# Optimization experiments

Hardware: AMD Instinct MI355X
Metric: run time of the kernel (lower is better)

Reference implementation:

```python
import jax, jax.numpy as jnp
import numpy as np

B = 8192
DV, DT = 1024, 768          # visual / text dims
H = 256                     # hidden_dim
C = 5                       # num_classes
GH = 128                    # gate_hidden_dim
K = 8                       # graph_k
ALPHA = 0.5                 # graph_alpha
EW = 0.01                   # entropy_weight
FD = 2 * H                  # fused_dim = 512
GI = FD + C + H             # gate input dim = 773
NEG = -1.0e9
LN_EPS = 1e-5
BN_EPS = 1e-5
N_IMAGES = 512


def setup_inputs() -> dict:
    key = jax.random.key(0)
    ks = jax.random.split(key, 20)
    def rn(k, sh, s=0.02):
        return jax.random.normal(k, sh, dtype=jnp.float32) * s
    # x = [visual(1024) | text(768) | bbox_ctx(4) | img_uid(1)]
    xf = jax.random.normal(ks[0], (B, DV + DT), dtype=jnp.float32)
    bbox = jax.random.uniform(ks[1], (B, 4), dtype=jnp.float32)
    img = jax.random.randint(ks[2], (B, 1), 0, N_IMAGES).astype(jnp.float32)
    x = jnp.concatenate([xf, bbox, img], axis=1)  # [B, 1797]
    return {
        "x": x,
        "ln_v_g": jnp.ones((DV,), jnp.float32), "ln_v_b": jnp.zeros((DV,), jnp.float32),
        "ln_t_g": jnp.ones((DT,), jnp.float32), "ln_t_b": jnp.zeros((DT,), jnp.float32),
        "W_v": rn(ks[3], (DV, H)), "b_v": jnp.zeros((H,), jnp.float32),
        "W_t": rn(ks[4], (DT, H)), "b_t": jnp.zeros((H,), jnp.float32),
        "W_cp": rn(ks[5], (FD, C)), "b_cp": jnp.zeros((C,), jnp.float32),
        "W_ctx1": rn(ks[6], (FD, H)), "b_ctx1": jnp.zeros((H,), jnp.float32),
        "W_ctx2": rn(ks[7], (H, H)), "b_ctx2": jnp.zeros((H,), jnp.float32),
        "W_g1": rn(ks[8], (GI, GH)), "b_g1": jnp.zeros((GH,), jnp.float32),
        "W_g2": rn(ks[9], (GH, 2)), "b_g2": jnp.zeros((2,), jnp.float32),
        "W_gu1": rn(ks[10], (FD, FD)), "b_gu1": jnp.zeros((FD,), jnp.float32),
        "W_gu2": rn(ks[11], (FD, FD)), "b_gu2": jnp.zeros((FD,), jnp.float32),
        "W_c1": rn(ks[12], (FD, H)), "b_c1": jnp.zeros((H,), jnp.float32),
        "bn_g": jnp.ones((H,), jnp.float32), "bn_b": jnp.zeros((H,), jnp.float32),
        "W_c2": rn(ks[13], (H, C)), "b_c2": jnp.zeros((C,), jnp.float32),
    }


def _layernorm(x, g, b):
    m = jnp.mean(x, axis=-1, keepdims=True)
    v = jnp.mean((x - m) ** 2, axis=-1, keepdims=True)
    return (x - m) * jax.lax.rsqrt(v + LN_EPS) * g + b


def _knn_aggregate(features, coords, img):
    """KNN over 2D spatial coords with same-image masking; softmax-weighted gather."""
    n = features.shape[0]
    sq = jnp.sum(coords * coords, axis=1)
    d2 = sq[:, None] + sq[None, :] - 2.0 * (coords @ coords.T)
    sim = -jnp.sqrt(jnp.clip(d2, 0.0))                 # [B, B] = -cdist
    eye = jnp.eye(n, dtype=bool)
    same = (img[None, :] == img[:, None]) & ~eye
    has_neighbor = jnp.any(same, axis=1)
    sim_same = jnp.where(same, sim, NEG)
    sim = jnp.where(has_neighbor[:, None], sim_same, sim)
    sim = jnp.where(eye, NEG, sim)
    vals, idx = jax.lax.top_k(sim, K)                  # [B, K]
    w = jax.nn.softmax(vals, axis=1)
    return jnp.einsum('bk,bkd->bd', w, features[idx])  # gather + weighted sum


def reference(x, ln_v_g, ln_v_b, ln_t_g, ln_t_b, W_v, b_v, W_t, b_t,
              W_cp, b_cp, W_ctx1, b_ctx1, W_ctx2, b_ctx2,
              W_g1, b_g1, W_g2, b_g2, W_gu1, b_gu1, W_gu2, b_gu2,
              W_c1, b_c1, bn_g, bn_b, W_c2, b_c2):
    xv = x[:, 0:DV]
    xt = x[:, DV:DV + DT]
    coords = x[:, DV + DT:DV + DT + 2]     # bbox_ctx[:, :2]
    img = x[:, DV + DT + 4]                # img_uid[:, 0]

    fv = _layernorm(xv, ln_v_g, ln_v_b) @ W_v + b_v
    ft = _layernorm(xt, ln_t_g, ln_t_b) @ W_t + b_t
    base_fused = jnp.concatenate([fv, ft], axis=1)     # [B, FD]

    class_prior = jax.lax.stop_gradient(jax.nn.softmax(base_fused @ W_cp + b_cp, axis=1))

    neigh_agg = _knn_aggregate(base_fused, coords, img)
    spatial_token = jax.nn.relu(neigh_agg @ W_ctx1 + b_ctx1) @ W_ctx2 + b_ctx2
    spatial_token = jax.lax.stop_gradient(spatial_token)

    gate_in = jnp.concatenate([base_fused, class_prior, spatial_token], axis=1)
    gate_logits = jax.nn.relu(gate_in @ W_g1 + b_g1) @ W_g2 + b_g2
    gate_probs = jax.nn.softmax(gate_logits / 1.0, axis=1)  # temperature=1.0 (eval: dropout off)
    entropy = -jnp.sum(gate_probs * jnp.log(gate_probs + 1e-8), axis=1)
    entropy_loss = jnp.mean(entropy) * EW

    fused = jnp.concatenate([fv * gate_probs[:, 0:1], ft * gate_probs[:, 1:2]], axis=1)
    spatial_update = _knn_aggregate(fused, coords, img)
    upd = jax.nn.relu(spatial_update @ W_gu1 + b_gu1) @ W_gu2 + b_gu2
    fused = fused + ALPHA * upd

    h = fused @ W_c1 + b_c1
    # eval-mode BatchNorm1d: running_mean=0, running_var=1
    h = h * (bn_g / jnp.sqrt(1.0 + BN_EPS)) + bn_b
    h = jax.nn.relu(h)
    logits = h @ W_c2 + b_c2
    return logits, entropy_loss
```

## Files before the change

kernel.cpp:

```cpp
#include <hip/hip_runtime.h>
#include <math.h>

#define B_ROWS 8192
#define DV_DIM 1024
#define DT_DIM 768
#define H_DIM 256
#define C_CLS 5
#define GH_DIM 128
#define K_NN 8
#define FD_DIM 512
#define GIP_DIM 832
#define GI_REAL 773
#define XCOLS 1797
#define NEGV -1000000000.0f
#define LN_EPS_F 1e-5f
#define BN_EPS_F 1e-5f
#define N_IMG 512
#define EW_F 0.01f
#define ALPHA_F 0.5f

typedef __attribute__((ext_vector_type(8))) short short8v;
typedef __attribute__((ext_vector_type(4))) float f32x4;

__device__ inline short bf16r(float f) {
    unsigned u = __float_as_uint(f);
    return (short)((u + 0x7fffu + ((u >> 16) & 1u)) >> 16);
}

__device__ inline float bf2f(short s) {
    return __uint_as_float(((unsigned)(unsigned short)s) << 16);
}

__device__ inline void split2(float f, short* h, short* l) {
    unsigned u = __float_as_uint(f);
    unsigned uh = (u + 0x7fffu + ((u >> 16) & 1u)) >> 16;
    float fh = __uint_as_float(uh << 16);
    float fl = f - fh;
    unsigned ul = __float_as_uint(fl);
    *h = (short)uh;
    *l = (short)((ul + 0x7fffu + ((ul >> 16) & 1u)) >> 16);
}

struct PrepArgs {
    const float* W[8];
    short* h[8];
    int K[8];
    int N[8];
    int Kpad[8];
    int cnt[8];
};

__global__ void prep_all_kernel(PrepArgs a, const float* __restrict__ x,
                                float* __restrict__ cx, float* __restrict__ cy,
                                float* __restrict__ sq, int* __restrict__ imgi,
                                int* __restrict__ cnt) {
    int idx = blockIdx.x * blockDim.x + threadIdx.x;
#pragma unroll
    for (int s = 0; s < 8; ++s) {
        if (idx < a.cnt[s]) {
            int Kp = a.Kpad[s];
            int n = idx / Kp, k = idx - n * Kp;
            float f = (k < a.K[s]) ? a.W[s][(size_t)k * a.N[s] + n] : 0.f;
            a.h[s][idx] = bf16r(f);
            return;
        }
        idx -= a.cnt[s];
    }
    if (idx < B_ROWS) {
        const float* row = x + (size_t)idx * XCOLS;
        float av = row[DV_DIM + DT_DIM];
        float bv = row[DV_DIM + DT_DIM + 1];
        cx[idx] = av; cy[idx] = bv; sq[idx] = av * av + bv * bv;
        int m = (int)row[DV_DIM + DT_DIM + 4];
        imgi[idx] = m;
        atomicAdd(&cnt[m], 1);
    }
}

__global__ void scan_kernel(const int* __restrict__ cnt, int* __restrict__ start,
                            int* __restrict__ cursor) {
    __shared__ int s[N_IMG];
    int t = threadIdx.x;
    s[t] = cnt[t];
    __syncthreads();
    for (int off = 1; off < N_IMG; off <<= 1) {
        int v = (t >= off) ? s[t - off] : 0;
        __syncthreads();
        s[t] += v;
        __syncthreads();
    }
    int st = s[t] - cnt[t];
    start[t] = st;
    cursor[t] = st;
}

__global__ void scatter_kernel(const int* __restrict__ imgi, int* __restrict__ cursor,
                               int* __restrict__ perm) {
    int i = blockIdx.x * blockDim.x + threadIdx.x;
    if (i >= B_ROWS) return;
    int pos = atomicAdd(&cursor[imgi[i]], 1);
    perm[pos] = i;
}

__global__ void knn_kernel(const float* __restrict__ cx, const float* __restrict__ cy,
                           const float* __restrict__ sq, const int* __restrict__ imgi,
                           const int* __restrict__ cnt, const int* __restrict__ start,
                           const int* __restrict__ perm, int* __restrict__ knn_idx,
                           float* __restrict__ knn_w) {
    int i = blockIdx.x * blockDim.x + threadIdx.x;
    if (i >= B_ROWS) return;
    float xi = cx[i], yi = cy[i], si = sq[i];
    float vals[K_NN];
    int ids[K_NN];
#pragma unroll
    for (int k = 0; k < K_NN; ++k) { vals[k] = NEGV; ids[k] = i; }
    int m = imgi[i];
    int s = cnt[m];
    if (s >= 2) {
        int st = start[m];
        for (int t = 0; t < s; ++t) {
            int j = perm[st + t];
            if (j == i) continue;
            float d2 = si + sq[j] - 2.f * (xi * cx[j] + yi * cy[j]);
            d2 = fmaxf(d2, 0.f);
            float v = -sqrtf(d2);
            if (v > vals[K_NN - 1]) {
                int p = K_NN - 1;
                while (p > 0 && vals[p - 1] < v) {
                    vals[p] = vals[p - 1]; ids[p] = ids[p - 1]; --p;
                }
                vals[p] = v; ids[p] = j;
            }
        }
    } else {
        for (int j = 0; j < B_ROWS; ++j) {
            if (j == i) continue;
            float d2 = si + sq[j] - 2.f * (xi * cx[j] + yi * cy[j]);
            d2 = fmaxf(d2, 0.f);
            float v = -sqrtf(d2);
            if (v > vals[K_NN - 1]) {
                int p = K_NN - 1;
                while (p > 0 && vals[p - 1] < v) {
                    vals[p] = vals[p - 1]; ids[p] = ids[p - 1]; --p;
                }
                vals[p] = v; ids[p] = j;
            }
        }
    }
    float mx = vals[0];
    float e[K_NN];
    float sum = 0.f;
#pragma unroll
    for (int k = 0; k < K_NN; ++k) { e[k] = expf(vals[k] - mx); sum += e[k]; }
    float inv = 1.f / sum;
#pragma unroll
    for (int k = 0; k < K_NN; ++k) {
        knn_w[(size_t)i * K_NN + k] = e[k] * inv;
        knn_idx[(size_t)i * K_NN + k] = ids[k];
    }
}

__global__ __launch_bounds__(256) void ln_split_kernel(
    const float* __restrict__ x,
    const float* __restrict__ gv, const float* __restrict__ bv,
    const float* __restrict__ gt, const float* __restrict__ bt,
    short* __restrict__ xvh, short* __restrict__ xvl,
    short* __restrict__ xth, short* __restrict__ xtl) {
    int row = blockIdx.x;
    int t = threadIdx.x;
    const float* xr = x + (size_t)row * XCOLS;
    __shared__ float red[256];

    float v[4];
#pragma unroll
    for (int k = 0; k < 4; ++k) v[k] = xr[t + k * 256];
    float sum = v[0] + v[1] + v[2] + v[3];
    red[t] = sum;
    __syncthreads();
    for (int off = 128; off; off >>= 1) {
        if (t < off) red[t] += red[t + off];
        __syncthreads();
    }
    float mean = red[0] * (1.f / DV_DIM);
    __syncthreads();
    float vs = 0.f;
#pragma unroll
    for (int k = 0; k < 4; ++k) { float d = v[k] - mean; vs += d * d; }
    red[t] = vs;
    __syncthreads();
    for (int off = 128; off; off >>= 1) {
        if (t < off) red[t] += red[t + off];
        __syncthreads();
    }
    float rs = rsqrtf(red[0] * (1.f / DV_DIM) + LN_EPS_F);
#pragma unroll
    for (int k = 0; k < 4; ++k) {
        int j = t + k * 256;
        float y = (v[k] - mean) * rs * gv[j] + bv[j];
        split2(y, &xvh[(size_t)row * DV_DIM + j], &xvl[(size_t)row * DV_DIM + j]);
    }
    __syncthreads();

    float u[3];
#pragma unroll
    for (int k = 0; k < 3; ++k) u[k] = xr[DV_DIM + t + k * 256];
    sum = u[0] + u[1] + u[2];
    red[t] = sum;
    __syncthreads();
    for (int off = 128; off; off >>= 1) {
        if (t < off) red[t] += red[t + off];
        __syncthreads();
    }
    mean = red[0] * (1.f / DT_DIM);
    __syncthreads();
    vs = 0.f;
#pragma unroll
    for (int k = 0; k < 3; ++k) { float d = u[k] - mean; vs += d * d; }
    red[t] = vs;
    __syncthreads();
    for (int off = 128; off; off >>= 1) {
        if (t < off) red[t] += red[t + off];
        __syncthreads();
    }
    rs = rsqrtf(red[0] * (1.f / DT_DIM) + LN_EPS_F);
#pragma unroll
    for (int k = 0; k < 3; ++k) {
        int j = t + k * 256;
        float y = (u[k] - mean) * rs * gt[j] + bt[j];
        split2(y, &xth[(size_t)row * DT_DIM + j], &xtl[(size_t)row * DT_DIM + j]);
    }
}

__device__ inline int xcd_swz(int wg, int nwg) {
    int q = nwg >> 3, r = nwg & 7;
    int xc = wg & 7, ii = wg >> 3;
    return (xc < r ? xc * (q + 1) : r * (q + 1) + (xc - r) * q) + ii;
}

struct GemmPair {
    const short* Ah; const short* Al;
    const short* Bh; const short* Bl;
    const float* bias;
    int K; int ncb; int colOff;
};

template <int MODE, int NPROD, int NF>
__global__ __launch_bounds__(256) void gemm2_kernel(
    GemmPair P0, GemmPair P1, int nblk0,
    float* __restrict__ Cf, short* __restrict__ Ch,
    int ldc, const float* __restrict__ aux1, const float* __restrict__ aux2) {
    constexpr int ASZ = 4096;
    constexpr int BSZ = 32 * NF * 64;
    constexpr int LDSZ = (NPROD == 3) ? 2 * (ASZ + BSZ) : (NPROD == 2 ? 2 * ASZ + BSZ : ASZ + BSZ);
    __shared__ short lds[LDSZ];
    short* sAh = lds;
    short* sAl = lds + ASZ;
    short* sBh = lds + ((NPROD >= 2) ? 2 * ASZ : ASZ);
    short* sBl = sBh + BSZ;

    const int tid = threadIdx.x;
    const int lane = tid & 63;
    const int wave = tid >> 6;
    const int wm = wave >> 1, wn = wave & 1;
    const int l15 = lane & 15, lq = lane >> 4;

    int wid = xcd_swz(blockIdx.x, gridDim.x);
    GemmPair G = P0;
    if (wid >= nblk0) { G = P1; wid -= nblk0; }

    const int panel = wid / G.ncb, cb = wid - panel * G.ncb;
    const long rowBase = (long)panel * 64;
    const int colBase = cb * (32 * NF);
    const int K = G.K;

    f32x4 acc[2][NF];
#pragma unroll
    for (int i = 0; i < 2; ++i)
#pragma unroll
        for (int j = 0; j < NF; ++j) acc[i][j] = (f32x4){0.f, 0.f, 0.f, 0.f};

    short8v pAh[2], pAl[2], pBh[NF], pBl[NF];
    const int ar0 = tid >> 3, ac = tid & 7;
    const int ar1 = (tid + 256) >> 3;

    {
        long go0 = (rowBase + ar0) * K + ac * 8;
        long go1 = (rowBase + ar1) * K + ac * 8;
        pAh[0] = *(const short8v*)(G.Ah + go0);
        pAh[1] = *(const short8v*)(G.Ah + go1);
        if constexpr (NPROD >= 2) {
            pAl[0] = *(const short8v*)(G.Al + go0);
            pAl[1] = *(const short8v*)(G.Al + go1);
        }
#pragma unroll
        for (int j = 0; j < NF; ++j) {
            int cid = tid + 256 * j;
            int cl = cid >> 3, c = cid & 7;
            long go = (colBase + cl) * (long)K + c * 8;
            pBh[j] = *(const short8v*)(G.Bh + go);
            if constexpr (NPROD == 3) pBl[j] = *(const short8v*)(G.Bl + go);
        }
    }

    const int nsteps = K >> 6;
    for (int s = 0; s < nsteps; ++s) {
        __syncthreads();
        {
            int off0 = ar0 * 64 + ((ac ^ (ar0 & 7)) << 3);
            int off1 = ar1 * 64 + ((ac ^ (ar1 & 7)) << 3);
            *(short8v*)(sAh + off0) = pAh[0];
            *(short8v*)(sAh + off1) = pAh[1];
            if constexpr (NPROD >= 2) {
                *(short8v*)(sAl + off0) = pAl[0];
                *(short8v*)(sAl + off1) = pAl[1];
            }
#pragma unroll
            for (int j = 0; j < NF; ++j) {
                int cid = tid + 256 * j;
                int cl = cid >> 3, c = cid & 7;
                int off = cl * 64 + ((c ^ (cl & 7)) << 3);
                *(short8v*)(sBh + off) = pBh[j];
                if constexpr (NPROD == 3) *(short8v*)(sBl + off) = pBl[j];
            }
        }
        __syncthreads();
        if (s + 1 < nsteps) {
            long ko = (long)(s + 1) * 64;
            long go0 = (rowBase + ar0) * K + ko + ac * 8;
            long go1 = (rowBase + ar1) * K + ko + ac * 8;
            pAh[0] = *(const short8v*)(G.Ah + go0);
            pAh[1] = *(const short8v*)(G.Ah + go1);
            if constexpr (NPROD >= 2) {
                pAl[0] = *(const short8v*)(G.Al + go0);
                pAl[1] = *(const short8v*)(G.Al + go1);
            }
#pragma unroll
            for (int j = 0; j < NF; ++j) {
                int cid = tid + 256 * j;
                int cl = cid >> 3, c = cid & 7;
                long go = (colBase + cl) * (long)K + ko + c * 8;
                pBh[j] = *(const short8v*)(G.Bh + go);
                if constexpr (NPROD == 3) pBl[j] = *(const short8v*)(G.Bl + go);
            }
        }
#pragma unroll
        for (int ksub = 0; ksub < 2; ++ksub) {
            int cc = ksub * 4 + lq;
            short8v afh[2], afl[2], bfh[NF], bfl[NF];
#pragma unroll
            for (int mf = 0; mf < 2; ++mf) {
                int rr = wm * 32 + mf * 16 + l15;
                int off = rr * 64 + ((cc ^ (rr & 7)) << 3);
                afh[mf] = *(short8v*)(sAh + off);
                if constexpr (NPROD >= 2) afl[mf] = *(short8v*)(sAl + off);
            }
#pragma unroll
            for (int nf = 0; nf < NF; ++nf) {
                int cl = wn * (NF * 16) + nf * 16 + l15;
                int off = cl * 64 + ((cc ^ (cl & 7)) << 3);
                bfh[nf] = *(short8v*)(sBh + off);
                if constexpr (NPROD == 3) bfl[nf] = *(short8v*)(sBl + off);
            }
#pragma unroll
            for (int mf = 0; mf < 2; ++mf)
#pragma unroll
                for (int nf = 0; nf < NF; ++nf) {
                    acc[mf][nf] = __builtin_amdgcn_mfma_f32_16x16x32_bf16(afh[mf], bfh[nf], acc[mf][nf], 0, 0, 0);
                    if constexpr (NPROD >= 2)
                        acc[mf][nf] = __builtin_amdgcn_mfma_f32_16x16x32_bf16(afl[mf], bfh[nf], acc[mf][nf], 0, 0, 0);
                    if constexpr (NPROD == 3)
                        acc[mf][nf] = __builtin_amdgcn_mfma_f32_16x16x32_bf16(afh[mf], bfl[nf], acc[mf][nf], 0, 0, 0);
                }
        }
    }

#pragma unroll
    for (int mf = 0; mf < 2; ++mf)
#pragma unroll
        for (int nf = 0; nf < NF; ++nf) {
            int col = colBase + wn * (NF * 16) + nf * 16 + l15;
            long row0 = rowBase + wm * 32 + mf * 16 + lq * 4;
#pragma unroll
            for (int rr = 0; rr < 4; ++rr) {
                long row = row0 + rr;
                float v = acc[mf][nf][rr] + G.bias[col];
                long o = row * ldc + G.colOff + col;
                if (MODE == 6) {
                    Cf[o] = v;
                    Ch[o] = bf16r(v);
                } else if (MODE == 3) {
                    Ch[o] = bf16r(fmaxf(v, 0.f));
                } else {
                    float g = aux2[row * 2 + (col >= H_DIM ? 1 : 0)];
                    float fv = aux1[row * FD_DIM + col] * g + ALPHA_F * v;
                    Ch[o] = bf16r(fv);
                }
            }
        }
}

__global__ __launch_bounds__(256) void post_base_kernel(
    const short* __restrict__ baseh, const float* __restrict__ Wcp,
    const float* __restrict__ bcp, const int* __restrict__ kidx,
    const float* __restrict__ wgt, short* __restrict__ gih,
    short* __restrict__ aggh) {
    int row = blockIdx.x;
    int t = threadIdx.x;
    short sa = baseh[(size_t)row * FD_DIM + t];
    short sb = baseh[(size_t)row * FD_DIM + t + 256];
    float a = bf2f(sa), b = bf2f(sb);

    __shared__ float red[C_CLS][256];
#pragma unroll
    for (int n = 0; n < C_CLS; ++n)
        red[n][t] = a * Wcp[t * C_CLS + n] + b * Wcp[(t + 256) * C_CLS + n];
    __syncthreads();
    for (int off = 128; off; off >>= 1) {
        if (t < off) {
#pragma unroll
            for (int n = 0; n < C_CLS; ++n) red[n][t] += red[n][t + off];
        }
        __syncthreads();
    }
    size_t go = (size_t)row * GIP_DIM;
    if (t == 0) {
        float lg[C_CLS];
#pragma unroll
        for (int n = 0; n < C_CLS; ++n) lg[n] = red[n][0] + bcp[n];
        float mx = lg[0];
#pragma unroll
        for (int n = 1; n < C_CLS; ++n) mx = fmaxf(mx, lg[n]);
        float s = 0.f;
        float e[C_CLS];
#pragma unroll
        for (int n = 0; n < C_CLS; ++n) { e[n] = expf(lg[n] - mx); s += e[n]; }
        float inv = 1.f / s;
#pragma unroll
        for (int n = 0; n < C_CLS; ++n) gih[go + FD_DIM + n] = bf16r(e[n] * inv);
    }
    gih[go + t] = sa;
    gih[go + t + 256] = sb;
    if (t < GIP_DIM - GI_REAL) gih[go + GI_REAL + t] = 0;

    int jj[K_NN];
    float ww[K_NN];
#pragma unroll
    for (int k = 0; k < K_NN; ++k) {
        jj[k] = kidx[(size_t)row * K_NN + k];
        ww[k] = wgt[(size_t)row * K_NN + k];
    }
#pragma unroll
    for (int half = 0; half < 2; ++half) {
        int d = t + half * 256;
        float s = 0.f;
#pragma unroll
        for (int k = 0; k < K_NN; ++k)
            s = fmaf(ww[k], bf2f(baseh[(size_t)jj[k] * FD_DIM + d]), s);
        aggh[(size_t)row * FD_DIM + d] = bf16r(s);
    }
}

__global__ __launch_bounds__(256) void gather_gate_kernel(
    const short* __restrict__ baseh, const int* __restrict__ kidx,
    const float* __restrict__ wgt, const float* __restrict__ gp,
    short* __restrict__ oh) {
    int row = blockIdx.x;
    int t = threadIdx.x;
    int jj[K_NN];
    float ww[K_NN], g0[K_NN], g1[K_NN];
#pragma unroll
    for (int k = 0; k < K_NN; ++k) {
        jj[k] = kidx[(size_t)row * K_NN + k];
        ww[k] = wgt[(size_t)row * K_NN + k];
        g0[k] = gp[(size_t)jj[k] * 2 + 0];
        g1[k] = gp[(size_t)jj[k] * 2 + 1];
    }
#pragma unroll
    for (int half = 0; half < 2; ++half) {
        int d = t + half * 256;
        float s = 0.f;
#pragma unroll
        for (int k = 0; k < K_NN; ++k) {
            float f = bf2f(baseh[(size_t)jj[k] * FD_DIM + d]);
            f *= (d < H_DIM) ? g0[k] : g1[k];
            s = fmaf(ww[k], f, s);
        }
        oh[(size_t)row * FD_DIM + d] = bf16r(s);
    }
}

__global__ __launch_bounds__(256) void ctxfused_kernel(
    const short* __restrict__ aggh, const short* __restrict__ wx1, const float* __restrict__ b1,
    const short* __restrict__ wx2, const float* __restrict__ b2, short* __restrict__ gih) {
    __shared__ short lds[2048 + 16384 + 8192];
    short* sA = lds;
    short* sB = lds + 2048;
    short* sH = lds + 2048 + 16384;

    const int tid = threadIdx.x;
    const int lane = tid & 63;
    const int wave = tid >> 6;
    const int l15 = lane & 15, lq = lane >> 4;
    int panel = xcd_swz(blockIdx.x, gridDim.x);
    const long rowBase = (long)panel * 32;

    const int ar = tid >> 3, ac = tid & 7;

    f32x4 acc[2][4];
#pragma unroll
    for (int i = 0; i < 2; ++i)
#pragma unroll
        for (int j = 0; j < 4; ++j) acc[i][j] = (f32x4){0.f, 0.f, 0.f, 0.f};

    short8v pA, pB[8];
    {
        pA = *(const short8v*)(aggh + (rowBase + ar) * 512 + ac * 8);
#pragma unroll
        for (int j = 0; j < 8; ++j) {
            int cid = tid + 256 * j;
            int cl = cid >> 3, c = cid & 7;
            pB[j] = *(const short8v*)(wx1 + (long)cl * 512 + c * 8);
        }
    }
    for (int s = 0; s < 8; ++s) {
        __syncthreads();
        *(short8v*)(sA + ar * 64 + ((ac ^ (ar & 7)) << 3)) = pA;
#pragma unroll
        for (int j = 0; j < 8; ++j) {
            int cid = tid + 256 * j;
            int cl = cid >> 3, c = cid & 7;
            *(short8v*)(sB + cl * 64 + ((c ^ (cl & 7)) << 3)) = pB[j];
        }
        __syncthreads();
        if (s + 1 < 8) {
            long ko = (long)(s + 1) * 64;
            pA = *(const short8v*)(aggh + (rowBase + ar) * 512 + ko + ac * 8);
#pragma unroll
            for (int j = 0; j < 8; ++j) {
                int cid = tid + 256 * j;
                int cl = cid >> 3, c = cid & 7;
                pB[j] = *(const short8v*)(wx1 + (long)cl * 512 + ko + c * 8);
            }
        }
#pragma unroll
        for (int ksub = 0; ksub < 2; ++ksub) {
            int cc = ksub * 4 + lq;
            short8v af[2], bf[4];
#pragma unroll
            for (int mf = 0; mf < 2; ++mf) {
                int rr = mf * 16 + l15;
                af[mf] = *(short8v*)(sA + rr * 64 + ((cc ^ (rr & 7)) << 3));
            }
#pragma unroll
            for (int nf = 0; nf < 4; ++nf) {
                int cl = wave * 64 + nf * 16 + l15;
                bf[nf] = *(short8v*)(sB + cl * 64 + ((cc ^ (cl & 7)) << 3));
            }
#pragma unroll
            for (int mf = 0; mf < 2; ++mf)
#pragma unroll
                for (int nf = 0; nf < 4; ++nf)
                    acc[mf][nf] = __builtin_amdgcn_mfma_f32_16x16x32_bf16(af[mf], bf[nf], acc[mf][nf], 0, 0, 0);
        }
    }
    __syncthreads();
#pragma unroll
    for (int mf = 0; mf < 2; ++mf)
#pragma unroll
        for (int nf = 0; nf < 4; ++nf) {
            int col = wave * 64 + nf * 16 + l15;
            int sub = col >> 6, cch = (col >> 3) & 7, ce = col & 7;
#pragma unroll
            for (int rr = 0; rr < 4; ++rr) {
                int r = mf * 16 + lq * 4 + rr;
                float v = fmaxf(acc[mf][nf][rr] + b1[col], 0.f);
                sH[sub * 2048 + r * 64 + ((cch ^ (r & 7)) << 3) + ce] = bf16r(v);
            }
        }
    f32x4 acc2[2][4];
#pragma unroll
    for (int i = 0; i < 2; ++i)
#pragma unroll
        for (int j = 0; j < 4; ++j) acc2[i][j] = (f32x4){0.f, 0.f, 0.f, 0.f};
    for (int s = 0; s < 4; ++s) {
        __syncthreads();
#pragma unroll
        for (int j = 0; j < 8; ++j) {
            int cid = tid + 256 * j;
            int cl = cid >> 3, c = cid & 7;
            short8v b = *(const short8v*)(wx2 + (long)cl * 256 + s * 64 + c * 8);
            *(short8v*)(sB + cl * 64 + ((c ^ (cl & 7)) << 3)) = b;
        }
        __syncthreads();
#pragma unroll
        for (int ksub = 0; ksub < 2; ++ksub) {
            int cc = ksub * 4 + lq;
            short8v af[2], bf[4];
#pragma unroll
            for (int mf = 0; mf < 2; ++mf) {
                int rr = mf * 16 + l15;
                af[mf] = *(short8v*)(sH + s * 2048 + rr * 64 + ((cc ^ (rr & 7)) << 3));
            }
#pragma unroll
            for (int nf = 0; nf < 4; ++nf) {
                int cl = wave * 64 + nf * 16 + l15;
                bf[nf] = *(short8v*)(sB + cl * 64 + ((cc ^ (cl & 7)) << 3));
            }
#pragma unroll
            for (int mf = 0; mf < 2; ++mf)
#pragma unroll
                for (int nf = 0; nf < 4; ++nf)
                    acc2[mf][nf] = __builtin_amdgcn_mfma_f32_16x16x32_bf16(af[mf], bf[nf], acc2[mf][nf], 0, 0, 0);
        }
    }
#pragma unroll
    for (int mf = 0; mf < 2; ++mf)
#pragma unroll
        for (int nf = 0; nf < 4; ++nf) {
            int col = wave * 64 + nf * 16 + l15;
#pragma unroll
            for (int rr = 0; rr < 4; ++rr) {
                long row = rowBase + mf * 16 + lq * 4 + rr;
                gih[row * GIP_DIM + FD_DIM + C_CLS + col] = bf16r(acc2[mf][nf][rr] + b2[col]);
            }
        }
}

__global__ __launch_bounds__(256) void g1gate_kernel(
    const short* __restrict__ gih, const short* __restrict__ wg1, const float* __restrict__ b1,
    const float* __restrict__ W2, const float* __restrict__ b2,
    float* __restrict__ gp, float* __restrict__ entpart) {
    __shared__ float hls[64 * 128];
    short* sA = (short*)hls;
    short* sB = sA + 4096;
    __shared__ float entrow[64];

    const int tid = threadIdx.x;
    const int lane = tid & 63;
    const int wave = tid >> 6;
    const int wm = wave >> 1, wn = wave & 1;
    const int l15 = lane & 15, lq = lane >> 4;
    int panel = xcd_swz(blockIdx.x, gridDim.x);
    const long rowBase = (long)panel * 64;

    const int ar0 = tid >> 3, ac = tid & 7;
    const int ar1 = (tid + 256) >> 3;
    constexpr int K = GIP_DIM;

    f32x4 acc[2][4];
#pragma unroll
    for (int i = 0; i < 2; ++i)
#pragma unroll
        for (int j = 0; j < 4; ++j) acc[i][j] = (f32x4){0.f, 0.f, 0.f, 0.f};

    short8v pA0, pA1, pB[4];
    {
        pA0 = *(const short8v*)(gih + (rowBase + ar0) * K + ac * 8);
        pA1 = *(const short8v*)(gih + (rowBase + ar1) * K + ac * 8);
#pragma unroll
        for (int j = 0; j < 4; ++j) {
            int cid = tid + 256 * j;
            int cl = cid >> 3, c = cid & 7;
            pB[j] = *(const short8v*)(wg1 + (long)cl * K + c * 8);
        }
    }
    const int nsteps = K >> 6;
    for (int s = 0; s < nsteps; ++s) {
        __syncthreads();
        *(short8v*)(sA + ar0 * 64 + ((ac ^ (ar0 & 7)) << 3)) = pA0;
        *(short8v*)(sA + ar1 * 64 + ((ac ^ (ar1 & 7)) << 3)) = pA1;
#pragma unroll
        for (int j = 0; j < 4; ++j) {
            int cid = tid + 256 * j;
            int cl = cid >> 3, c = cid & 7;
            *(short8v*)(sB + cl * 64 + ((c ^ (cl & 7)) << 3)) = pB[j];
        }
        __syncthreads();
        if (s + 1 < nsteps) {
            long ko = (long)(s + 1) * 64;
            pA0 = *(const short8v*)(gih + (rowBase + ar0) * K + ko + ac * 8);
            pA1 = *(const short8v*)(gih + (rowBase + ar1) * K + ko + ac * 8);
#pragma unroll
            for (int j = 0; j < 4; ++j) {
                int cid = tid + 256 * j;
                int cl = cid >> 3, c = cid & 7;
                pB[j] = *(const short8v*)(wg1 + (long)cl * K + ko + c * 8);
            }
        }
#pragma unroll
        for (int ksub = 0; ksub < 2; ++ksub) {
            int cc = ksub * 4 + lq;
            short8v af[2], bf[4];
#pragma unroll
            for (int mf = 0; mf < 2; ++mf) {
                int rr = wm * 32 + mf * 16 + l15;
                af[mf] = *(short8v*)(sA + rr * 64 + ((cc ^ (rr & 7)) << 3));
            }
#pragma unroll
            for (int nf = 0; nf < 4; ++nf) {
                int cl = wn * 64 + nf * 16 + l15;
                bf[nf] = *(short8v*)(sB + cl * 64 + ((cc ^ (cl & 7)) << 3));
            }
#pragma unroll
            for (int mf = 0; mf < 2; ++mf)
#pragma unroll
                for (int nf = 0; nf < 4; ++nf)
                    acc[mf][nf] = __builtin_amdgcn_mfma_f32_16x16x32_bf16(af[mf], bf[nf], acc[mf][nf], 0, 0, 0);
        }
    }
    __syncthreads();
#pragma unroll
    for (int mf = 0; mf < 2; ++mf)
#pragma unroll
        for (int nf = 0; nf < 4; ++nf) {
            int col = wn * 64 + nf * 16 + l15;
#pragma unroll
            for (int rr = 0; rr < 4; ++rr) {
                int r = wm * 32 + mf * 16 + lq * 4 + rr;
                hls[r * 128 + col] = fmaxf(acc[mf][nf][rr] + b1[col], 0.f);
            }
        }
    __syncthreads();
    {
        int r = tid >> 2, p = tid & 3;
        float a0 = 0.f, a1 = 0.f;
#pragma unroll
        for (int i = 0; i < 32; ++i) {
            int c = p + i * 4;
            float hv = hls[r * 128 + c];
            a0 = fmaf(hv, W2[c * 2 + 0], a0);
            a1 = fmaf(hv, W2[c * 2 + 1], a1);
        }
        a0 += __shfl_xor(a0, 1); a1 += __shfl_xor(a1, 1);
        a0 += __shfl_xor(a0, 2); a1 += __shfl_xor(a1, 2);
        if (p == 0) {
            float l0 = a0 + b2[0], l1 = a1 + b2[1];
            float mx = fmaxf(l0, l1);
            float e0 = expf(l0 - mx), e1 = expf(l1 - mx);
            float ssum = e0 + e1;
            float p0 = e0 / ssum, p1 = e1 / ssum;
            long grow = rowBase + r;
            gp[grow * 2 + 0] = p0;
            gp[grow * 2 + 1] = p1;
            entrow[r] = -(p0 * logf(p0 + 1e-8f) + p1 * logf(p1 + 1e-8f));
        }
    }
    __syncthreads();
    if (tid == 0) {
        float s = 0.f;
        for (int r = 0; r < 64; ++r) s += entrow[r];
        entpart[blockIdx.x] = s;
    }
}

__global__ __launch_bounds__(256) void c1logits_kernel(
    const short* __restrict__ fusedh, const short* __restrict__ wc1, const float* __restrict__ b1,
    const float* __restrict__ bng, const float* __restrict__ bnb,
    const float* __restrict__ W2, const float* __restrict__ b2,
    const float* __restrict__ entpart, float* __restrict__ out) {
    __shared__ short lds[2048 + 16384];
    short* sA = lds;
    short* sB = lds + 2048;
    float* hls = (float*)lds;

    const int tid = threadIdx.x;
    const int lane = tid & 63;
    const int wave = tid >> 6;
    const int l15 = lane & 15, lq = lane >> 4;
    int panel = xcd_swz(blockIdx.x, gridDim.x);
    const long rowBase = (long)panel * 32;
    const int ar = tid >> 3, ac = tid & 7;

    f32x4 acc[2][4];
#pragma unroll
    for (int i = 0; i < 2; ++i)
#pragma unroll
        for (int j = 0; j < 4; ++j) acc[i][j] = (f32x4){0.f, 0.f, 0.f, 0.f};

    short8v pA, pB[8];
    {
        pA = *(const short8v*)(fusedh + (rowBase + ar) * 512 + ac * 8);
#pragma unroll
        for (int j = 0; j < 8; ++j) {
            int cid = tid + 256 * j;
            int cl = cid >> 3, c = cid & 7;
            pB[j] = *(const short8v*)(wc1 + (long)cl * 512 + c * 8);
        }
    }
    for (int s = 0; s < 8; ++s) {
        __syncthreads();
        *(short8v*)(sA + ar * 64 + ((ac ^ (ar & 7)) << 3)) = pA;
#pragma unroll
        for (int j = 0; j < 8; ++j) {
            int cid = tid + 256 * j;
            int cl = cid >> 3, c = cid & 7;
            *(short8v*)(sB + cl * 64 + ((c ^ (cl & 7)) << 3)) = pB[j];
        }
        __syncthreads();
        if (s + 1 < 8) {
            long ko = (long)(s + 1) * 64;
            pA = *(const short8v*)(fusedh + (rowBase + ar) * 512 + ko + ac * 8);
#pragma unroll
            for (int j = 0; j < 8; ++j) {
                int cid = tid + 256 * j;
                int cl = cid >> 3, c = cid & 7;
                pB[j] = *(const short8v*)(wc1 + (long)cl * 512 + ko + c * 8);
            }
        }
#pragma unroll
        for (int ksub = 0; ksub < 2; ++ksub) {
            int cc = ksub * 4 + lq;
            short8v af[2], bf[4];
#pragma unroll
            for (int mf = 0; mf < 2; ++mf) {
                int rr = mf * 16 + l15;
                af[mf] = *(short8v*)(sA + rr * 64 + ((cc ^ (rr & 7)) << 3));
            }
#pragma unroll
            for (int nf = 0; nf < 4; ++nf) {
                int cl = wave * 64 + nf * 16 + l15;
                bf[nf] = *(short8v*)(sB + cl * 64 + ((cc ^ (cl & 7)) << 3));
            }
#pragma unroll
            for (int mf = 0; mf < 2; ++mf)
#pragma unroll
                for (int nf = 0; nf < 4; ++nf)
                    acc[mf][nf] = __builtin_amdgcn_mfma_f32_16x16x32_bf16(af[mf], bf[nf], acc[mf][nf], 0, 0, 0);
        }
    }
    __syncthreads();
#pragma unroll
    for (int mf = 0; mf < 2; ++mf)
#pragma unroll
        for (int nf = 0; nf < 4; ++nf) {
            int col = wave * 64 + nf * 16 + l15;
            float scale = bng[col] * rsqrtf(1.f + BN_EPS_F);
            float shift = bnb[col];
#pragma unroll
            for (int rr = 0; rr < 4; ++rr) {
                int r = mf * 16 + lq * 4 + rr;
                float v = (acc[mf][nf][rr] + b1[col]) * scale + shift;
                hls[r * 256 + col] = fmaxf(v, 0.f);
            }
        }
    __syncthreads();
    {
        int r = tid >> 3, p = tid & 7;
        float a[C_CLS];
#pragma unroll
        for (int n = 0; n < C_CLS; ++n) a[n] = 0.f;
#pragma unroll
        for (int i = 0; i < 32; ++i) {
            int c = p + i * 8;
            float hv = hls[r * 256 + c];
#pragma unroll
            for (int n = 0; n < C_CLS; ++n) a[n] = fmaf(hv, W2[c * 5 + n], a[n]);
        }
#pragma unroll
        for (int n = 0; n < C_CLS; ++n) {
            a[n] += __shfl_xor(a[n], 1);
            a[n] += __shfl_xor(a[n], 2);
            a[n] += __shfl_xor(a[n], 4);
        }
        if (p == 0) {
            long grow = rowBase + r;
#pragma unroll
            for (int n = 0; n < C_CLS; ++n) out[grow * C_CLS + n] = a[n] + b2[n];
        }
    }
    if (blockIdx.x == 0 && tid < 64) {
        float s = entpart[tid] + entpart[tid + 64];
        for (int off = 32; off; off >>= 1) s += __shfl_down(s, off);
        if (tid == 0) out[(size_t)B_ROWS * C_CLS] = s * (EW_F / (float)B_ROWS);
    }
}

extern "C" void kernel_launch(void* const* d_in, const int* in_sizes, int n_in,
                              void* d_out, int out_size, void* d_ws, size_t ws_size,
                              hipStream_t stream) {
    const float* x = (const float*)d_in[0];
    const float* ln_v_g = (const float*)d_in[1];
    const float* ln_v_b = (const float*)d_in[2];
    const float* ln_t_g = (const float*)d_in[3];
    const float* ln_t_b = (const float*)d_in[4];
    const float* W_v = (const float*)d_in[5];
    const float* b_v = (const float*)d_in[6];
    const float* W_t = (const float*)d_in[7];
    const float* b_t = (const float*)d_in[8];
    const float* W_cp = (const float*)d_in[9];
    const float* b_cp = (const float*)d_in[10];
    const float* W_ctx1 = (const float*)d_in[11];
    const float* b_ctx1 = (const float*)d_in[12];
    const float* W_ctx2 = (const float*)d_in[13];
    const float* b_ctx2 = (const float*)d_in[14];
    const float* W_g1 = (const float*)d_in[15];
    const float* b_g1 = (const float*)d_in[16];
    const float* W_g2 = (const float*)d_in[17];
    const float* b_g2 = (const float*)d_in[18];
    const float* W_gu1 = (const float*)d_in[19];
    const float* b_gu1 = (const float*)d_in[20];
    const float* W_gu2 = (const float*)d_in[21];
    const float* b_gu2 = (const float*)d_in[22];
    const float* W_c1 = (const float*)d_in[23];
    const float* b_c1 = (const float*)d_in[24];
    const float* bn_g = (const float*)d_in[25];
    const float* bn_b = (const float*)d_in[26];
    const float* W_c2 = (const float*)d_in[27];
    const float* b_c2 = (const float*)d_in[28];

    float* out = (float*)d_out;

    char* wsb = (char*)d_ws;
    size_t off = 0;
    auto alloc = [&](size_t bytes) {
        char* p = wsb + off;
        off += (bytes + 255) & ~(size_t)255;
        return p;
    };
    float* base = (float*)alloc((size_t)B_ROWS * FD_DIM * 4);
    short* baseh = (short*)alloc((size_t)B_ROWS * FD_DIM * 2);
    short* aggh = (short*)alloc((size_t)B_ROWS * FD_DIM * 2);
    float* gp = (float*)alloc((size_t)B_ROWS * 2 * 4);
    float* entpart = (float*)alloc(128 * 4);
    float* cxv = (float*)alloc((size_t)B_ROWS * 4);
    float* cyv = (float*)alloc((size_t)B_ROWS * 4);
    float* sqv = (float*)alloc((size_t)B_ROWS * 4);
    float* wgt = (float*)alloc((size_t)B_ROWS * K_NN * 4);
    int* imgi = (int*)alloc((size_t)B_ROWS * 4);
    int* cnt = (int*)alloc(N_IMG * 4);
    int* startb = (int*)alloc(N_IMG * 4);
    int* cursor = (int*)alloc(N_IMG * 4);
    int* perm = (int*)alloc((size_t)B_ROWS * 4);
    int* kidx = (int*)alloc((size_t)B_ROWS * K_NN * 4);
    short* wv_h = (short*)alloc(256 * 1024 * 2);
    short* wt_h = (short*)alloc(256 * 768 * 2);
    short* wx1_h = (short*)alloc(256 * 512 * 2);
    short* wx2_h = (short*)alloc(256 * 256 * 2);
    short* wg1_h = (short*)alloc(128 * GIP_DIM * 2);
    short* wu1_h = (short*)alloc(512 * 512 * 2);
    short* wu2_h = (short*)alloc(512 * 512 * 2);
    short* wc1_h = (short*)alloc(256 * 512 * 2);
    char* R = alloc((size_t)B_ROWS * (DV_DIM + DT_DIM) * 2 * 2);
    short* xvh = (short*)R;
    short* xvl = xvh + (size_t)B_ROWS * DV_DIM;
    short* xth = xvl + (size_t)B_ROWS * DV_DIM;
    short* xtl = xth + (size_t)B_ROWS * DT_DIM;
    short* gih = (short*)R;
    short* guh = gih + (size_t)B_ROWS * GIP_DIM;
    short* fusedh = aggh;

    dim3 blk(256);
    dim3 gridRows((B_ROWS + 255) / 256);

    PrepArgs pa;
    const float* pw[8] = {W_v, W_t, W_ctx1, W_ctx2, W_g1, W_gu1, W_gu2, W_c1};
    short* ph[8] = {wv_h, wt_h, wx1_h, wx2_h, wg1_h, wu1_h, wu2_h, wc1_h};
    int pK[8] = {1024, 768, 512, 256, GI_REAL, 512, 512, 512};
    int pN[8] = {256, 256, 256, 256, 128, 512, 512, 256};
    int pKp[8] = {1024, 768, 512, 256, GIP_DIM, 512, 512, 512};
    int total = 0;
    for (int s = 0; s < 8; ++s) {
        pa.W[s] = pw[s]; pa.h[s] = ph[s];
        pa.K[s] = pK[s]; pa.N[s] = pN[s]; pa.Kpad[s] = pKp[s];
        pa.cnt[s] = pN[s] * pKp[s];
        total += pa.cnt[s];
    }
    hipMemsetAsync(cnt, 0, N_IMG * sizeof(int), stream);
    prep_all_kernel<<<(total + B_ROWS + 255) / 256, blk, 0, stream>>>(
        pa, x, cxv, cyv, sqv, imgi, cnt);

    scan_kernel<<<1, N_IMG, 0, stream>>>(cnt, startb, cursor);
    scatter_kernel<<<gridRows, blk, 0, stream>>>(imgi, cursor, perm);
    knn_kernel<<<gridRows, blk, 0, stream>>>(cxv, cyv, sqv, imgi, cnt, startb, perm, kidx, wgt);

    ln_split_kernel<<<B_ROWS, blk, 0, stream>>>(x, ln_v_g, ln_v_b, ln_t_g, ln_t_b,
                                                xvh, xvl, xth, xtl);

    GemmPair fvP{xvh, xvl, wv_h, nullptr, b_v, 1024, 4, 0};
    GemmPair ftP{xth, xtl, wt_h, nullptr, b_t, 768, 4, 256};
    gemm2_kernel<6, 2, 2><<<1024, blk, 0, stream>>>(fvP, ftP, 512, base, baseh,
                                                    FD_DIM, nullptr, nullptr);

    post_base_kernel<<<B_ROWS, blk, 0, stream>>>(baseh, W_cp, b_cp, kidx, wgt, gih, aggh);

    ctxfused_kernel<<<256, blk, 0, stream>>>(aggh, wx1_h, b_ctx1, wx2_h, b_ctx2, gih);

    g1gate_kernel<<<128, blk, 0, stream>>>(gih, wg1_h, b_g1, W_g2, b_g2, gp, entpart);

    gather_gate_kernel<<<B_ROWS, blk, 0, stream>>>(baseh, kidx, wgt, gp, aggh);
    GemmPair u1P{aggh, nullptr, wu1_h, nullptr, b_gu1, 512, 4, 0};
    gemm2_kernel<3, 1, 4><<<512, blk, 0, stream>>>(u1P, u1P, 512, nullptr, guh,
                                                   FD_DIM, nullptr, nullptr);
    GemmPair u2P{guh, nullptr, wu2_h, nullptr, b_gu2, 512, 4, 0};
    gemm2_kernel<5, 1, 4><<<512, blk, 0, stream>>>(u2P, u2P, 512, nullptr, fusedh,
                                                   FD_DIM, base, gp);

    c1logits_kernel<<<256, blk, 0, stream>>>(fusedh, wc1_h, b_c1, bn_g, bn_b,
                                             W_c2, b_c2, entpart, out);

    (void)in_sizes; (void)n_in; (void)out_size; (void)ws_size;
}
```

Baseline: 201.7 us.

## Drop bf16 split-precision for input GEMM and fuse kNN into LayerNorm launch

LayerNorm outputs are now stored as a single bf16 value instead of a hi/lo pair, and the first GEMM runs one MFMA product per tile instead of two. This halves the activation write/read traffic and the MFMA work for the largest GEMM. The kNN search is also folded into the LayerNorm kernel as 32 extra blocks, saving one launch and letting the two overlap. The price is lower precision in the visual and text projections, which could push outputs past the tolerance.

```diff
diff --git a/kernel.cpp b/kernel.cpp
--- a/kernel.cpp
+++ b/kernel.cpp
@@ -31,16 +31,6 @@
     return __uint_as_float(((unsigned)(unsigned short)s) << 16);
 }
 
-__device__ inline void split2(float f, short* h, short* l) {
-    unsigned u = __float_as_uint(f);
-    unsigned uh = (u + 0x7fffu + ((u >> 16) & 1u)) >> 16;
-    float fh = __uint_as_float(uh << 16);
-    float fl = f - fh;
-    unsigned ul = __float_as_uint(fl);
-    *h = (short)uh;
-    *l = (short)((ul + 0x7fffu + ((ul >> 16) & 1u)) >> 16);
-}
-
 struct PrepArgs {
     const float* W[8];
     short* h[8];
@@ -102,70 +92,70 @@
     perm[pos] = i;
 }
 
-__global__ void knn_kernel(const float* __restrict__ cx, const float* __restrict__ cy,
-                           const float* __restrict__ sq, const int* __restrict__ imgi,
-                           const int* __restrict__ cnt, const int* __restrict__ start,
-                           const int* __restrict__ perm, int* __restrict__ knn_idx,
-                           float* __restrict__ knn_w) {
-    int i = blockIdx.x * blockDim.x + threadIdx.x;
-    if (i >= B_ROWS) return;
-    float xi = cx[i], yi = cy[i], si = sq[i];
-    float vals[K_NN];
-    int ids[K_NN];
-#pragma unroll
-    for (int k = 0; k < K_NN; ++k) { vals[k] = NEGV; ids[k] = i; }
-    int m = imgi[i];
-    int s = cnt[m];
-    if (s >= 2) {
-        int st = start[m];
-        for (int t = 0; t < s; ++t) {
-            int j = perm[st + t];
-            if (j == i) continue;
-            float d2 = si + sq[j] - 2.f * (xi * cx[j] + yi * cy[j]);
-            d2 = fmaxf(d2, 0.f);
-            float v = -sqrtf(d2);
-            if (v > vals[K_NN - 1]) {
-                int p = K_NN - 1;
-                while (p > 0 && vals[p - 1] < v) {
-                    vals[p] = vals[p - 1]; ids[p] = ids[p - 1]; --p;
-                }
-                vals[p] = v; ids[p] = j;
-            }
-        }
-    } else {
-        for (int j = 0; j < B_ROWS; ++j) {
-            if (j == i) continue;
-            float d2 = si + sq[j] - 2.f * (xi * cx[j] + yi * cy[j]);
-            d2 = fmaxf(d2, 0.f);
-            float v = -sqrtf(d2);
-            if (v > vals[K_NN - 1]) {
-                int p = K_NN - 1;
-                while (p > 0 && vals[p - 1] < v) {
-                    vals[p] = vals[p - 1]; ids[p] = ids[p - 1]; --p;
-                }
-                vals[p] = v; ids[p] = j;
-            }
-        }
-    }
-    float mx = vals[0];
-    float e[K_NN];
-    float sum = 0.f;
-#pragma unroll
-    for (int k = 0; k < K_NN; ++k) { e[k] = expf(vals[k] - mx); sum += e[k]; }
-    float inv = 1.f / sum;
-#pragma unroll
-    for (int k = 0; k < K_NN; ++k) {
-        knn_w[(size_t)i * K_NN + k] = e[k] * inv;
-        knn_idx[(size_t)i * K_NN + k] = ids[k];
-    }
-}
-
-__global__ __launch_bounds__(256) void ln_split_kernel(
+__global__ __launch_bounds__(256) void lnknn_kernel(
     const float* __restrict__ x,
     const float* __restrict__ gv, const float* __restrict__ bv,
     const float* __restrict__ gt, const float* __restrict__ bt,
-    short* __restrict__ xvh, short* __restrict__ xvl,
-    short* __restrict__ xth, short* __restrict__ xtl) {
+    short* __restrict__ xvh, short* __restrict__ xth,
+    const float* __restrict__ cx, const float* __restrict__ cy,
+    const float* __restrict__ sq, const int* __restrict__ imgi,
+    const int* __restrict__ cnt, const int* __restrict__ start,
+    const int* __restrict__ perm, int* __restrict__ knn_idx,
+    float* __restrict__ knn_w) {
+    if (blockIdx.x >= B_ROWS) {
+        int i = (blockIdx.x - B_ROWS) * 256 + threadIdx.x;
+        if (i >= B_ROWS) return;
+        float xi = cx[i], yi = cy[i], si = sq[i];
+        float vals[K_NN];
+        int ids[K_NN];
+#pragma unroll
+        for (int k = 0; k < K_NN; ++k) { vals[k] = NEGV; ids[k] = i; }
+        int m = imgi[i];
+        int s = cnt[m];
+        if (s >= 2) {
+            int st = start[m];
+            for (int t = 0; t < s; ++t) {
+                int j = perm[st + t];
+                if (j == i) continue;
+                float d2 = si + sq[j] - 2.f * (xi * cx[j] + yi * cy[j]);
+                d2 = fmaxf(d2, 0.f);
+                float v = -sqrtf(d2);
+                if (v > vals[K_NN - 1]) {
+                    int p = K_NN - 1;
+                    while (p > 0 && vals[p - 1] < v) {
+                        vals[p] = vals[p - 1]; ids[p] = ids[p - 1]; --p;
+                    }
+                    vals[p] = v; ids[p] = j;
+                }
+            }
+        } else {
+            for (int j = 0; j < B_ROWS; ++j) {
+                if (j == i) continue;
+                float d2 = si + sq[j] - 2.f * (xi * cx[j] + yi * cy[j]);
+                d2 = fmaxf(d2, 0.f);
+                float v = -sqrtf(d2);
+                if (v > vals[K_NN - 1]) {
+                    int p = K_NN - 1;
+                    while (p > 0 && vals[p - 1] < v) {
+                        vals[p] = vals[p - 1]; ids[p] = ids[p - 1]; --p;
+                    }
+                    vals[p] = v; ids[p] = j;
+                }
+            }
+        }
+        float mx = vals[0];
+        float e[K_NN];
+        float sum = 0.f;
+#pragma unroll
+        for (int k = 0; k < K_NN; ++k) { e[k] = expf(vals[k] - mx); sum += e[k]; }
+        float inv = 1.f / sum;
+#pragma unroll
+        for (int k = 0; k < K_NN; ++k) {
+            knn_w[(size_t)i * K_NN + k] = e[k] * inv;
+            knn_idx[(size_t)i * K_NN + k] = ids[k];
+        }
+        return;
+    }
     int row = blockIdx.x;
     int t = threadIdx.x;
     const float* xr = x + (size_t)row * XCOLS;
@@ -197,7 +187,7 @@
     for (int k = 0; k < 4; ++k) {
         int j = t + k * 256;
         float y = (v[k] - mean) * rs * gv[j] + bv[j];
-        split2(y, &xvh[(size_t)row * DV_DIM + j], &xvl[(size_t)row * DV_DIM + j]);
+        xvh[(size_t)row * DV_DIM + j] = bf16r(y);
     }
     __syncthreads();
 
@@ -227,7 +217,7 @@
     for (int k = 0; k < 3; ++k) {
         int j = t + k * 256;
         float y = (u[k] - mean) * rs * gt[j] + bt[j];
-        split2(y, &xth[(size_t)row * DT_DIM + j], &xtl[(size_t)row * DT_DIM + j]);
+        xth[(size_t)row * DT_DIM + j] = bf16r(y);
     }
 }
 
@@ -239,7 +229,7 @@
 
 struct GemmPair {
     const short* Ah; const short* Al;
-    const short* Bh; const short* Bl;
+    const short* Bh;
     const float* bias;
     int K; int ncb; int colOff;
 };
@@ -251,12 +241,11 @@
     int ldc, const float* __restrict__ aux1, const float* __restrict__ aux2) {
     constexpr int ASZ = 4096;
     constexpr int BSZ = 32 * NF * 64;
-    constexpr int LDSZ = (NPROD == 3) ? 2 * (ASZ + BSZ) : (NPROD == 2 ? 2 * ASZ + BSZ : ASZ + BSZ);
+    constexpr int LDSZ = (NPROD == 2) ? 2 * ASZ + BSZ : ASZ + BSZ;
     __shared__ short lds[LDSZ];
     short* sAh = lds;
     short* sAl = lds + ASZ;
-    short* sBh = lds + ((NPROD >= 2) ? 2 * ASZ : ASZ);
-    short* sBl = sBh + BSZ;
+    short* sBh = lds + ((NPROD == 2) ? 2 * ASZ : ASZ);
 
     const int tid = threadIdx.x;
     const int lane = tid & 63;
@@ -279,7 +268,7 @@
 #pragma unroll
         for (int j = 0; j < NF; ++j) acc[i][j] = (f32x4){0.f, 0.f, 0.f, 0.f};
 
-    short8v pAh[2], pAl[2], pBh[NF], pBl[NF];
+    short8v pAh[2], pAl[2], pBh[NF];
     const int ar0 = tid >> 3, ac = tid & 7;
     const int ar1 = (tid + 256) >> 3;
 
@@ -288,7 +277,7 @@
         long go1 = (rowBase + ar1) * K + ac * 8;
         pAh[0] = *(const short8v*)(G.Ah + go0);
         pAh[1] = *(const short8v*)(G.Ah + go1);
-        if constexpr (NPROD >= 2) {
+        if constexpr (NPROD == 2) {
             pAl[0] = *(const short8v*)(G.Al + go0);
             pAl[1] = *(const short8v*)(G.Al + go1);
         }
@@ -298,7 +287,6 @@
             int cl = cid >> 3, c = cid & 7;
             long go = (colBase + cl) * (long)K + c * 8;
             pBh[j] = *(const short8v*)(G.Bh + go);
-            if constexpr (NPROD == 3) pBl[j] = *(const short8v*)(G.Bl + go);
         }
     }
 
@@ -310,7 +298,7 @@
             int off1 = ar1 * 64 + ((ac ^ (ar1 & 7)) << 3);
             *(short8v*)(sAh + off0) = pAh[0];
             *(short8v*)(sAh + off1) = pAh[1];
-            if constexpr (NPROD >= 2) {
+            if constexpr (NPROD == 2) {
                 *(short8v*)(sAl + off0) = pAl[0];
                 *(short8v*)(sAl + off1) = pAl[1];
             }
@@ -320,7 +308,6 @@
                 int cl = cid >> 3, c = cid & 7;
                 int off = cl * 64 + ((c ^ (cl & 7)) << 3);
                 *(short8v*)(sBh + off) = pBh[j];
-                if constexpr (NPROD == 3) *(short8v*)(sBl + off) = pBl[j];
             }
         }
         __syncthreads();
@@ -330,7 +317,7 @@
             long go1 = (rowBase + ar1) * K + ko + ac * 8;
             pAh[0] = *(const short8v*)(G.Ah + go0);
             pAh[1] = *(const short8v*)(G.Ah + go1);
-            if constexpr (NPROD >= 2) {
+            if constexpr (NPROD == 2) {
                 pAl[0] = *(const short8v*)(G.Al + go0);
                 pAl[1] = *(const short8v*)(G.Al + go1);
             }
@@ -340,36 +327,32 @@
                 int cl = cid >> 3, c = cid & 7;
                 long go = (colBase + cl) * (long)K + ko + c * 8;
                 pBh[j] = *(const short8v*)(G.Bh + go);
-                if constexpr (NPROD == 3) pBl[j] = *(const short8v*)(G.Bl + go);
             }
         }
 #pragma unroll
         for (int ksub = 0; ksub < 2; ++ksub) {
             int cc = ksub * 4 + lq;
-            short8v afh[2], afl[2], bfh[NF], bfl[NF];
+            short8v afh[2], afl[2], bfh[NF];
 #pragma unroll
             for (int mf = 0; mf < 2; ++mf) {
                 int rr = wm * 32 + mf * 16 + l15;
                 int off = rr * 64 + ((cc ^ (rr & 7)) << 3);
                 afh[mf] = *(short8v*)(sAh + off);
-                if constexpr (NPROD >= 2) afl[mf] = *(short8v*)(sAl + off);
+                if constexpr (NPROD == 2) afl[mf] = *(short8v*)(sAl + off);
             }
 #pragma unroll
             for (int nf = 0; nf < NF; ++nf) {
                 int cl = wn * (NF * 16) + nf * 16 + l15;
                 int off = cl * 64 + ((cc ^ (cl & 7)) << 3);
                 bfh[nf] = *(short8v*)(sBh + off);
-                if constexpr (NPROD == 3) bfl[nf] = *(short8v*)(sBl + off);
             }
 #pragma unroll
             for (int mf = 0; mf < 2; ++mf)
 #pragma unroll
                 for (int nf = 0; nf < NF; ++nf) {
                     acc[mf][nf] = __builtin_amdgcn_mfma_f32_16x16x32_bf16(afh[mf], bfh[nf], acc[mf][nf], 0, 0, 0);
-                    if constexpr (NPROD >= 2)
+                    if constexpr (NPROD == 2)
                         acc[mf][nf] = __builtin_amdgcn_mfma_f32_16x16x32_bf16(afl[mf], bfh[nf], acc[mf][nf], 0, 0, 0);
-                    if constexpr (NPROD == 3)
-                        acc[mf][nf] = __builtin_amdgcn_mfma_f32_16x16x32_bf16(afh[mf], bfl[nf], acc[mf][nf], 0, 0, 0);
                 }
         }
     }
@@ -942,9 +925,7 @@
     short* wc1_h = (short*)alloc(256 * 512 * 2);
     char* R = alloc((size_t)B_ROWS * (DV_DIM + DT_DIM) * 2 * 2);
     short* xvh = (short*)R;
-    short* xvl = xvh + (size_t)B_ROWS * DV_DIM;
-    short* xth = xvl + (size_t)B_ROWS * DV_DIM;
-    short* xtl = xth + (size_t)B_ROWS * DT_DIM;
+    short* xth = xvh + (size_t)B_ROWS * DV_DIM;
     short* gih = (short*)R;
     short* guh = gih + (size_t)B_ROWS * GIP_DIM;
     short* fusedh = aggh;
@@ -971,14 +952,14 @@
 
     scan_kernel<<<1, N_IMG, 0, stream>>>(cnt, startb, cursor);
     scatter_kernel<<<gridRows, blk, 0, stream>>>(imgi, cursor, perm);
-    knn_kernel<<<gridRows, blk, 0, stream>>>(cxv, cyv, sqv, imgi, cnt, startb, perm, kidx, wgt);
-
-    ln_split_kernel<<<B_ROWS, blk, 0, stream>>>(x, ln_v_g, ln_v_b, ln_t_g, ln_t_b,
-                                                xvh, xvl, xth, xtl);
-
-    GemmPair fvP{xvh, xvl, wv_h, nullptr, b_v, 1024, 4, 0};
-    GemmPair ftP{xth, xtl, wt_h, nullptr, b_t, 768, 4, 256};
-    gemm2_kernel<6, 2, 2><<<1024, blk, 0, stream>>>(fvP, ftP, 512, base, baseh,
+
+    lnknn_kernel<<<B_ROWS + 32, blk, 0, stream>>>(
+        x, ln_v_g, ln_v_b, ln_t_g, ln_t_b, xvh, xth,
+        cxv, cyv, sqv, imgi, cnt, startb, perm, kidx, wgt);
+
+    GemmPair fvP{xvh, nullptr, wv_h, b_v, 1024, 4, 0};
+    GemmPair ftP{xth, nullptr, wt_h, b_t, 768, 4, 256};
+    gemm2_kernel<6, 1, 2><<<1024, blk, 0, stream>>>(fvP, ftP, 512, base, baseh,
                                                     FD_DIM, nullptr, nullptr);
 
     post_base_kernel<<<B_ROWS, blk, 0, stream>>>(baseh, W_cp, b_cp, kidx, wgt, gih, aggh);
@@ -988,10 +969,10 @@
     g1gate_kernel<<<128, blk, 0, stream>>>(gih, wg1_h, b_g1, W_g2, b_g2, gp, entpart);
 
     gather_gate_kernel<<<B_ROWS, blk, 0, stream>>>(baseh, kidx, wgt, gp, aggh);
-    GemmPair u1P{aggh, nullptr, wu1_h, nullptr, b_gu1, 512, 4, 0};
+    GemmPair u1P{aggh, nullptr, wu1_h, b_gu1, 512, 4, 0};
     gemm2_kernel<3, 1, 4><<<512, blk, 0, stream>>>(u1P, u1P, 512, nullptr, guh,
                                                    FD_DIM, nullptr, nullptr);
-    GemmPair u2P{guh, nullptr, wu2_h, nullptr, b_gu2, 512, 4, 0};
+    GemmPair u2P{guh, nullptr, wu2_h, b_gu2, 512, 4, 0};
     gemm2_kernel<5, 1, 4><<<512, blk, 0, stream>>>(u2P, u2P, 512, nullptr, fusedh,
                                                    FD_DIM, base, gp);
 
```

Result: faster. 187.9 us (-6.8%).
